# Optimization experiments

Hardware: AMD Instinct MI355X
Metric: run time of the kernel (lower is better)

Reference implementation:

```python
import jax, jax.numpy as jnp
import numpy as np

BETA = 1.0 / np.sqrt(768.0).astype(np.float32)


def setup_inputs() -> dict:
    key = jax.random.key(0)
    k1, k2, k3 = jax.random.split(key, 3)
    x = jax.random.normal(k1, (32, 512, 768), dtype=jnp.float32)
    # torch nn.Linear(dim, n_prototype).weight has shape [n_prototype, dim]
    w_lookup = jax.random.normal(k2, (4096, 768), dtype=jnp.float32) * 0.02
    # torch nn.Linear(n_prototype, dim).weight has shape [dim, n_prototype]
    w_content = jax.random.normal(k3, (768, 4096), dtype=jnp.float32) * 0.02
    return {"x": x, "w_lookup": w_lookup, "w_content": w_content}


def reference(x, w_lookup, w_content):
    # scores: [b, s, n_prototype] = x @ w_lookup^T, scaled by 1/sqrt(dim)
    scores = jnp.einsum("bsd,pd->bsp", x, w_lookup) * jnp.asarray(BETA, x.dtype)
    lookup = jax.nn.softmax(scores, axis=-1)
    # content: [b, s, dim] = lookup @ w_content^T
    content = jnp.einsum("bsp,dp->bsd", lookup, w_content)
    return content  # dropout is identity in eval / p=0.0
```

## Files before the change

### kernel.cpp

```cpp
#include <hip/hip_runtime.h>
#include <hip/hip_bf16.h>


#define NTOK   16384
#define DIM    768
#define NPROT  4096
#define BETA_F 0.03608439182428583f

typedef __bf16 bf16_t;
typedef __bf16 bf16x8 __attribute__((ext_vector_type(8)));
typedef float  floatx4 __attribute__((ext_vector_type(4)));

__device__ __forceinline__ void async_copy16(const bf16_t* g, void* l) {
  __builtin_amdgcn_global_load_lds(
      (__attribute__((address_space(1))) const void*)g,
      (__attribute__((address_space(3))) void*)l, 16, 0, 0);
}

__global__ __launch_bounds__(256) void cvt_all(
    const float* __restrict__ x, const float* __restrict__ wl,
    const float* __restrict__ wc, bf16_t* __restrict__ xb,
    bf16_t* __restrict__ wlb, bf16_t* __restrict__ wcb,
    int nx8, int nw8, int nc8) {
  int i = blockIdx.x * 256 + threadIdx.x;
  const float* in; bf16_t* out; int k;
  if (i < nx8)            { in = x;  out = xb;  k = i; }
  else if (i < nx8 + nw8) { in = wl; out = wlb; k = i - nx8; }
  else if (i < nx8 + nw8 + nc8) { in = wc; out = wcb; k = i - nx8 - nw8; }
  else return;
  const float4* in4 = (const float4*)in;
  float4 a = in4[2 * k], b = in4[2 * k + 1];
  bf16x8 o;
  o[0] = (bf16_t)a.x; o[1] = (bf16_t)a.y; o[2] = (bf16_t)a.z; o[3] = (bf16_t)a.w;
  o[4] = (bf16_t)b.x; o[5] = (bf16_t)b.y; o[6] = (bf16_t)b.z; o[7] = (bf16_t)b.w;
  ((bf16x8*)out)[k] = o;
}

__global__ __launch_bounds__(512, 2)
void gemm256(const bf16_t* __restrict__ A, const bf16_t* __restrict__ B,
             bf16_t* __restrict__ P, float* __restrict__ rowsum,
             const int K, const int N, const int nN) {
  __shared__ char lds[131072];

  const int tid = threadIdx.x;
  const int l   = tid & 63;
  const int w   = tid >> 6;
  const int wr  = w >> 2;
  const int wc  = w & 3;
  const int lr  = l & 15;
  const int lk  = (l >> 4) << 3;

  const int nwg   = gridDim.x;
  const int chunk = nwg >> 3;
  const int wg    = (blockIdx.x & 7) * chunk + (blockIdx.x >> 3);
  const int m0    = (wg / nN) * 256;
  const int n0    = (wg % nN) * 256;

  int aoff[2][2], boff[2][2];
#pragma unroll
  for (int h = 0; h < 2; ++h)
#pragma unroll
    for (int j = 0; j < 2; ++j) {
      const int s     = j * 8 + w;
      const int mfrag = h * 8 + (s >> 1);
      const int ks    = s & 1;
      aoff[h][j] = (m0 + mfrag * 16 + lr) * K + ks * 32 + lk;
      boff[h][j] = (n0 + mfrag * 16 + lr) * K + ks * 32 + lk;
    }

  auto stageA = [&](int slot, int kt, int h) {
#pragma unroll
    for (int j = 0; j < 2; ++j) {
      const int s  = j * 8 + w;
      const int sf = (h * 8 + (s >> 1)) * 2 + (s & 1);
      async_copy16(A + aoff[h][j] + kt * 64, lds + slot * 65536 + sf * 1024);
    }
  };
  auto stageB = [&](int slot, int kt, int h) {
#pragma unroll
    for (int j = 0; j < 2; ++j) {
      const int s  = j * 8 + w;
      const int sf = (h * 8 + (s >> 1)) * 2 + (s & 1);
      async_copy16(B + boff[h][j] + kt * 64,
                   lds + slot * 65536 + 32768 + sf * 1024);
    }
  };

  bf16x8 af[4][2], bg[4][2];
  auto loadA = [&](int slot, int mh) {
#pragma unroll
    for (int q = 0; q < 4; ++q)
#pragma unroll
      for (int ks = 0; ks < 2; ++ks)
        af[q][ks] = *(const bf16x8*)(lds + slot * 65536 +
                        ((mh * 8 + q * 2 + wr) * 2 + ks) * 1024 + l * 16);
  };
  auto loadB = [&](int slot, int nh, int qb) {
#pragma unroll
    for (int q = 0; q < 2; ++q)
#pragma unroll
      for (int ks = 0; ks < 2; ++ks)
        bg[qb + q][ks] = *(const bf16x8*)(lds + slot * 65536 + 32768 +
                        ((nh * 8 + q * 4 + wc) * 2 + ks) * 1024 + l * 16);
  };

  const floatx4 z = {0.f, 0.f, 0.f, 0.f};
  floatx4 acc[8][4];
#pragma unroll
  for (int mt = 0; mt < 8; ++mt)
#pragma unroll
    for (int nt = 0; nt < 4; ++nt) acc[mt][nt] = z;

  auto mma = [&](int mq, int nq) {
    __builtin_amdgcn_s_setprio(1);
#pragma unroll
    for (int q = 0; q < 4; ++q)
#pragma unroll
      for (int r = 0; r < 2; ++r)
#pragma unroll
        for (int ks = 0; ks < 2; ++ks)
          acc[mq * 4 + q][nq * 2 + r] = __builtin_amdgcn_mfma_f32_16x16x32_bf16(
              af[q][ks], bg[nq * 2 + r][ks], acc[mq * 4 + q][nq * 2 + r], 0, 0, 0);
    __builtin_amdgcn_s_setprio(0);
  };

#define BAR()    __builtin_amdgcn_s_barrier()
#define LGKM0()  asm volatile("s_waitcnt lgkmcnt(0)")
#define LGKM8()  asm volatile("s_waitcnt lgkmcnt(8)")
#define VM(n)    asm volatile("s_waitcnt vmcnt(" #n ")" ::: "memory")

  const int T = K >> 6;

  stageA(0, 0, 0); stageB(0, 0, 0); stageB(0, 0, 1); stageA(0, 0, 1);
  stageA(1, 1, 0); stageB(1, 1, 0); stageB(1, 1, 1);
  VM(6);
  BAR();

#pragma unroll 1
  for (int t = 0; t < T - 2; t += 2) {
    loadA(0, 0); loadB(0, 0, 0);
    stageA(1, t + 1, 1);
    LGKM8();
    BAR(); LGKM0(); mma(0, 0); BAR();
    loadB(0, 1, 2);
    stageA(0, t + 2, 0);
    BAR(); LGKM0(); mma(0, 1); BAR();
    loadA(0, 1);
    stageB(0, t + 2, 0);
    BAR(); LGKM0(); mma(1, 1); BAR();
    stageB(0, t + 2, 1);
    BAR(); mma(1, 0); VM(6); BAR();
    loadA(1, 0); loadB(1, 0, 0);
    stageA(0, t + 2, 1);
    LGKM8();
    BAR(); LGKM0(); mma(0, 0); BAR();
    loadB(1, 1, 2);
    stageA(1, t + 3, 0);
    BAR(); LGKM0(); mma(0, 1); BAR();
    loadA(1, 1);
    stageB(1, t + 3, 0);
    BAR(); LGKM0(); mma(1, 1); BAR();
    stageB(1, t + 3, 1);
    BAR(); mma(1, 0); VM(6); BAR();
  }

  loadA(0, 0); loadB(0, 0, 0);
  stageA(1, T - 1, 1);
  LGKM8();
  BAR(); LGKM0(); mma(0, 0); BAR();
  loadB(0, 1, 2);
  BAR(); LGKM0(); mma(0, 1); BAR();
  loadA(0, 1);
  BAR(); LGKM0(); mma(1, 1); BAR();
  BAR(); mma(1, 0); VM(0); BAR();
  loadA(1, 0); loadB(1, 0, 0);
  BAR(); LGKM0(); mma(0, 0); BAR();
  loadB(1, 1, 2);
  BAR(); LGKM0(); mma(0, 1); BAR();
  loadA(1, 1);
  BAR(); LGKM0(); mma(1, 1); BAR();
  mma(1, 0);

  const int hi4 = (l >> 4) << 2;
#pragma unroll
  for (int mt = 0; mt < 8; ++mt) {
    const int row = m0 + (mt * 2 + wr) * 16 + hi4;
    float rs[4] = {0.f, 0.f, 0.f, 0.f};
#pragma unroll
    for (int nt = 0; nt < 4; ++nt) {
      const int col = n0 + (nt * 4 + wc) * 16 + lr;
#pragma unroll
      for (int i = 0; i < 4; ++i) {
        const float e = __expf(acc[mt][nt][i] * BETA_F);
        P[(row + i) * N + col] = (bf16_t)e;
        rs[i] += e;
      }
    }
#pragma unroll
    for (int i = 0; i < 4; ++i) {
      float s = rs[i];
      s += __shfl_xor(s, 1);
      s += __shfl_xor(s, 2);
      s += __shfl_xor(s, 4);
      s += __shfl_xor(s, 8);
      if (lr == 0) atomicAdd(&rowsum[row + i], s);
    }
  }
}

__global__ __launch_bounds__(512, 2)
void gemm192(const bf16_t* __restrict__ A, const bf16_t* __restrict__ B,
             float* __restrict__ O, const float* __restrict__ rowsum,
             const int K, const int N) {
  __shared__ char lds[114688];

  const int tid = threadIdx.x;
  const int l   = tid & 63;
  const int w   = tid >> 6;
  const int wr  = w >> 2;
  const int wc  = w & 3;
  const int lr  = l & 15;
  const int lk  = (l >> 4) << 3;

  const int wg = (blockIdx.x & 7) * 32 + (blockIdx.x >> 3);
  const int m0 = (wg >> 2) * 256;
  const int n0 = (wg & 3) * 192;

  int aoff[2][2];
#pragma unroll
  for (int h = 0; h < 2; ++h)
#pragma unroll
    for (int j = 0; j < 2; ++j) {
      const int s     = j * 8 + w;
      const int mfrag = h * 8 + (s >> 1);
      const int ks    = s & 1;
      aoff[h][j] = (m0 + mfrag * 16 + lr) * K + ks * 32 + lk;
    }
  int boff[3];
#pragma unroll
  for (int t = 0; t < 3; ++t)
    boff[t] = (n0 + (t * 4 + (w >> 1)) * 16 + lr) * K + (w & 1) * 32 + lk;

  auto stageA = [&](int slot, int kt, int h) {
#pragma unroll
    for (int j = 0; j < 2; ++j) {
      const int s  = j * 8 + w;
      const int sf = (h * 8 + (s >> 1)) * 2 + (s & 1);
      async_copy16(A + aoff[h][j] + kt * 64, lds + slot * 57344 + sf * 1024);
    }
  };
  auto stageBt = [&](int slot, int kt, int t) {
    async_copy16(B + boff[t] + kt * 64,
                 lds + slot * 57344 + 32768 + (t * 8 + w) * 1024 + l * 16);
  };

  bf16x8 af[4][2], bg[3][2];
  auto loadA = [&](int slot, int mh) {
#pragma unroll
    for (int q = 0; q < 4; ++q)
#pragma unroll
      for (int ks = 0; ks < 2; ++ks)
        af[q][ks] = *(const bf16x8*)(lds + slot * 57344 +
                        ((mh * 8 + q * 2 + wr) * 2 + ks) * 1024 + l * 16);
  };
  auto loadBn = [&](int slot, int nlo, int ncnt) {
    for (int r = 0; r < ncnt; ++r)
#pragma unroll
      for (int ks = 0; ks < 2; ++ks)
        bg[nlo + r][ks] = *(const bf16x8*)(lds + slot * 57344 + 32768 +
                        (((wc * 3 + nlo + r) * 2 + ks) << 10) + l * 16);
  };

  const floatx4 z = {0.f, 0.f, 0.f, 0.f};
  floatx4 acc[8][3];
#pragma unroll
  for (int mt = 0; mt < 8; ++mt)
#pragma unroll
    for (int nt = 0; nt < 3; ++nt) acc[mt][nt] = z;

  auto mma = [&](int mq, int nlo, int ncnt) {
    __builtin_amdgcn_s_setprio(1);
#pragma unroll
    for (int q = 0; q < 4; ++q)
      for (int r = 0; r < ncnt; ++r)
#pragma unroll
        for (int ks = 0; ks < 2; ++ks)
          acc[mq * 4 + q][nlo + r] = __builtin_amdgcn_mfma_f32_16x16x32_bf16(
              af[q][ks], bg[nlo + r][ks], acc[mq * 4 + q][nlo + r], 0, 0, 0);
    __builtin_amdgcn_s_setprio(0);
  };

  const int T = K >> 6;

  stageA(0, 0, 0); stageA(0, 0, 1);
  stageBt(0, 0, 0); stageBt(0, 0, 1); stageBt(0, 0, 2);
  stageA(1, 1, 0);
  stageBt(1, 1, 0); stageBt(1, 1, 1); stageBt(1, 1, 2);
  VM(5);
  BAR();

#pragma unroll 1
  for (int t = 0; t < T - 2; t += 2) {
#pragma unroll
    for (int u = 0; u < 2; ++u) {
      const int p = u;
      loadA(p, 0); loadBn(p, 0, 2);
      stageA(p ^ 1, t + u + 1, 1);
      LGKM8();
      BAR(); LGKM0(); mma(0, 0, 2); BAR();
      loadBn(p, 2, 1);
      stageA(p, t + u + 2, 0);
      BAR(); LGKM0(); mma(0, 2, 1); BAR();
      loadA(p, 1);
      stageBt(p, t + u + 2, 0); stageBt(p, t + u + 2, 1);
      BAR(); LGKM0(); mma(1, 0, 2); BAR();
      stageBt(p, t + u + 2, 2);
      BAR(); mma(1, 2, 1); VM(5); BAR();
    }
  }

  loadA(0, 0); loadBn(0, 0, 2);
  stageA(1, T - 1, 1);
  LGKM8();
  BAR(); LGKM0(); mma(0, 0, 2); BAR();
  loadBn(0, 2, 1);
  BAR(); LGKM0(); mma(0, 2, 1); BAR();
  loadA(0, 1);
  BAR(); LGKM0(); mma(1, 0, 2); BAR();
  BAR(); mma(1, 2, 1); VM(0); BAR();
  loadA(1, 0); loadBn(1, 0, 2);
  BAR(); LGKM0(); mma(0, 0, 2); BAR();
  loadBn(1, 2, 1);
  BAR(); LGKM0(); mma(0, 2, 1); BAR();
  loadA(1, 1);
  BAR(); LGKM0(); mma(1, 0, 2); BAR();
  mma(1, 2, 1);

#undef BAR
#undef LGKM0
#undef LGKM8
#undef VM

  const int hi4 = (l >> 4) << 2;
#pragma unroll
  for (int mt = 0; mt < 8; ++mt) {
    const int row = m0 + (mt * 2 + wr) * 16 + hi4;
#pragma unroll
    for (int i = 0; i < 4; ++i) {
      const float inv = 1.0f / rowsum[row + i];
#pragma unroll
      for (int nt = 0; nt < 3; ++nt)
        O[(row + i) * N + n0 + (wc * 3 + nt) * 16 + lr] = acc[mt][nt][i] * inv;
    }
  }
}

__global__ __launch_bounds__(256) void hopfield_fallback(
    const float* __restrict__ x, const float* __restrict__ wl,
    const float* __restrict__ wc, float* __restrict__ out) {
  __shared__ float  xs[8 * 768];
  __shared__ bf16_t ps[8 * 4096];
  __shared__ float  rs[8];
  const int tid = threadIdx.x;
  const int r0  = blockIdx.x * 8;
  if (tid < 8) rs[tid] = 0.f;
  for (int i = tid; i < 8 * 768; i += 256)
    xs[i] = x[(r0 + (i / 768)) * 768 + (i % 768)];
  __syncthreads();

  float lsum[8] = {0, 0, 0, 0, 0, 0, 0, 0};
  for (int p = tid; p < 4096; p += 256) {
    float s[8] = {0, 0, 0, 0, 0, 0, 0, 0};
    for (int d = 0; d < 768; ++d) {
      const float wv = wl[p * 768 + d];
#pragma unroll
      for (int r = 0; r < 8; ++r) s[r] += xs[r * 768 + d] * wv;
    }
#pragma unroll
    for (int r = 0; r < 8; ++r) {
      const float e = __expf(s[r] * BETA_F);
      ps[r * 4096 + p] = (bf16_t)e;
      lsum[r] += e;
    }
  }
#pragma unroll
  for (int r = 0; r < 8; ++r) atomicAdd(&rs[r], lsum[r]);
  __syncthreads();

  for (int d = tid; d < 768; d += 256) {
    float o[8] = {0, 0, 0, 0, 0, 0, 0, 0};
    for (int p = 0; p < 4096; ++p) {
      const float wv = wc[d * 4096 + p];
#pragma unroll
      for (int r = 0; r < 8; ++r) o[r] += (float)ps[r * 4096 + p] * wv;
    }
#pragma unroll
    for (int r = 0; r < 8; ++r) out[(r0 + r) * 768 + d] = o[r] / rs[r];
  }
}

extern "C" void kernel_launch(void* const* d_in, const int* in_sizes, int n_in,
                              void* d_out, int out_size, void* d_ws, size_t ws_size,
                              hipStream_t stream) {
  (void)in_sizes; (void)n_in; (void)out_size;
  const float* x  = (const float*)d_in[0];
  const float* wl = (const float*)d_in[1];
  const float* wc = (const float*)d_in[2];
  float* out = (float*)d_out;

  const size_t xb_e = (size_t)NTOK * DIM;
  const size_t wl_e = (size_t)NPROT * DIM;
  const size_t wc_e = (size_t)DIM * NPROT;
  const size_t P_e  = (size_t)NTOK * NPROT;
  const size_t need = (xb_e + wl_e + wc_e + P_e) * 2 + (size_t)NTOK * 4;

  if (ws_size >= need) {
    char* ws = (char*)d_ws;
    bf16_t* xb  = (bf16_t*)ws;  ws += xb_e * 2;
    bf16_t* wlb = (bf16_t*)ws;  ws += wl_e * 2;
    bf16_t* wcb = (bf16_t*)ws;  ws += wc_e * 2;
    bf16_t* P   = (bf16_t*)ws;  ws += P_e * 2;
    float* rowsum = (float*)ws;

    hipMemsetAsync(rowsum, 0, NTOK * sizeof(float), stream);
    const int nx8 = (int)(xb_e / 8), nw8 = (int)(wl_e / 8), nc8 = (int)(wc_e / 8);
    cvt_all<<<(nx8 + nw8 + nc8 + 255) / 256, 256, 0, stream>>>(
        x, wl, wc, xb, wlb, wcb, nx8, nw8, nc8);
    gemm256<<<dim3((NTOK / 256) * (NPROT / 256)), 512, 0, stream>>>(
        xb, wlb, P, rowsum, DIM, NPROT, NPROT / 256);
    gemm192<<<dim3(256), 512, 0, stream>>>(
        P, wcb, out, rowsum, NPROT, DIM);
  } else {
    hopfield_fallback<<<NTOK / 8, 256, 0, stream>>>(x, wl, wc, out);
  }
}
```

Before: 415.0 us.

## Pre-tile bf16 operands into LDS fragment order during conversion for contiguous loads

The fp32-to-bf16 conversion kernel now writes x, w_lookup and w_content in a blocked layout that matches the per-tile LDS fragment order used by both GEMMs. Each async global-to-LDS copy then reads a contiguous 1 KB chunk per fragment instead of 16-byte pieces strided by K. The aim is better memory coalescing and fewer cache lines touched per stage, paid for with scattered writes in the conversion kernel. The layout bakes in the fixed dimensions and tile shapes.

```diff
diff --git a/kernel.cpp b/kernel.cpp
--- a/kernel.cpp
+++ b/kernel.cpp
@@ -23,17 +23,36 @@
     bf16_t* __restrict__ wlb, bf16_t* __restrict__ wcb,
     int nx8, int nw8, int nc8) {
   int i = blockIdx.x * 256 + threadIdx.x;
-  const float* in; bf16_t* out; int k;
-  if (i < nx8)            { in = x;  out = xb;  k = i; }
-  else if (i < nx8 + nw8) { in = wl; out = wlb; k = i - nx8; }
-  else if (i < nx8 + nw8 + nc8) { in = wc; out = wcb; k = i - nx8 - nw8; }
-  else return;
+  const float* in; bf16_t* out; int k; int dv;
+  if (i < nx8) {
+    in = x; out = xb; k = i;
+    const int m = k / 96, kv = k % 96;
+    const int kt = kv >> 3, kr = kv & 7;
+    const int sf = (((m >> 4) & 15) << 1) + (kr >> 2);
+    const int l  = (m & 15) + ((kr & 3) << 4);
+    dv = (((m >> 8) * 12 + kt) * 32 + sf) * 64 + l;
+  } else if (i < nx8 + nw8) {
+    in = wl; out = wlb; k = i - nx8;
+    const int p = k / 96, kv = k % 96;
+    const int kt = kv >> 3, kr = kv & 7;
+    const int sf = (((p >> 4) & 15) << 1) + (kr >> 2);
+    const int l  = (p & 15) + ((kr & 3) << 4);
+    dv = (((p >> 8) * 12 + kt) * 32 + sf) * 64 + l;
+  } else if (i < nx8 + nw8 + nc8) {
+    in = wc; out = wcb; k = i - nx8 - nw8;
+    const int d = k / 512, pv = k % 512;
+    const int kt = pv >> 3, kr = pv & 7;
+    const int dd = d % 192;
+    const int sf = ((dd >> 4) << 1) + (kr >> 2);
+    const int l  = (dd & 15) + ((kr & 3) << 4);
+    dv = (((d / 192) * 64 + kt) * 24 + sf) * 64 + l;
+  } else return;
   const float4* in4 = (const float4*)in;
   float4 a = in4[2 * k], b = in4[2 * k + 1];
   bf16x8 o;
   o[0] = (bf16_t)a.x; o[1] = (bf16_t)a.y; o[2] = (bf16_t)a.z; o[3] = (bf16_t)a.w;
   o[4] = (bf16_t)b.x; o[5] = (bf16_t)b.y; o[6] = (bf16_t)b.z; o[7] = (bf16_t)b.w;
-  ((bf16x8*)out)[k] = o;
+  ((bf16x8*)out)[dv] = o;
 }
 
 __global__ __launch_bounds__(512, 2)
@@ -48,7 +67,6 @@
   const int wr  = w >> 2;
   const int wc  = w & 3;
   const int lr  = l & 15;
-  const int lk  = (l >> 4) << 3;
 
   const int nwg   = gridDim.x;
   const int chunk = nwg >> 3;
@@ -56,16 +74,17 @@
   const int m0    = (wg / nN) * 256;
   const int n0    = (wg % nN) * 256;
 
-  int aoff[2][2], boff[2][2];
+  const int T = K >> 6;
+  const int abase = (m0 >> 8) * T * 16384 + l * 8;
+  const int bbase = (n0 >> 8) * T * 16384 + l * 8;
+  int asf[2][2], bsf[2][2];
 #pragma unroll
   for (int h = 0; h < 2; ++h)
 #pragma unroll
     for (int j = 0; j < 2; ++j) {
-      const int s     = j * 8 + w;
-      const int mfrag = h * 8 + (s >> 1);
-      const int ks    = s & 1;
-      aoff[h][j] = (m0 + mfrag * 16 + lr) * K + ks * 32 + lk;
-      boff[h][j] = (n0 + mfrag * 16 + lr) * K + ks * 32 + lk;
+      const int s = j * 8 + w;
+      asf[h][j] = ((h * 8 + (s >> 1)) * 2 + (s & 1)) * 512;
+      bsf[h][j] = asf[h][j];
     }
 
   auto stageA = [&](int slot, int kt, int h) {
@@ -73,7 +92,8 @@
     for (int j = 0; j < 2; ++j) {
       const int s  = j * 8 + w;
       const int sf = (h * 8 + (s >> 1)) * 2 + (s & 1);
-      async_copy16(A + aoff[h][j] + kt * 64, lds + slot * 65536 + sf * 1024);
+      async_copy16(A + abase + kt * 16384 + asf[h][j],
+                   lds + slot * 65536 + sf * 1024);
     }
   };
   auto stageB = [&](int slot, int kt, int h) {
@@ -81,7 +101,7 @@
     for (int j = 0; j < 2; ++j) {
       const int s  = j * 8 + w;
       const int sf = (h * 8 + (s >> 1)) * 2 + (s & 1);
-      async_copy16(B + boff[h][j] + kt * 64,
+      async_copy16(B + bbase + kt * 16384 + bsf[h][j],
                    lds + slot * 65536 + 32768 + sf * 1024);
     }
   };
@@ -128,8 +148,6 @@
 #define LGKM0()  asm volatile("s_waitcnt lgkmcnt(0)")
 #define LGKM8()  asm volatile("s_waitcnt lgkmcnt(8)")
 #define VM(n)    asm volatile("s_waitcnt vmcnt(" #n ")" ::: "memory")
-
-  const int T = K >> 6;
 
   stageA(0, 0, 0); stageB(0, 0, 0); stageB(0, 0, 1); stageA(0, 0, 1);
   stageA(1, 1, 0); stageB(1, 1, 0); stageB(1, 1, 1);
@@ -236,10 +254,10 @@
       const int ks    = s & 1;
       aoff[h][j] = (m0 + mfrag * 16 + lr) * K + ks * 32 + lk;
     }
-  int boff[3];
-#pragma unroll
-  for (int t = 0; t < 3; ++t)
-    boff[t] = (n0 + (t * 4 + (w >> 1)) * 16 + lr) * K + (w & 1) * 32 + lk;
+  const int bb = (n0 / 192) * 64 * 12288 + l * 8;
+  int bsf[3];
+#pragma unroll
+  for (int t = 0; t < 3; ++t) bsf[t] = (t * 8 + w) * 512;
 
   auto stageA = [&](int slot, int kt, int h) {
 #pragma unroll
@@ -250,7 +268,7 @@
     }
   };
   auto stageBt = [&](int slot, int kt, int t) {
-    async_copy16(B + boff[t] + kt * 64,
+    async_copy16(B + bb + kt * 12288 + bsf[t],
                  lds + slot * 57344 + 32768 + (t * 8 + w) * 1024 + l * 16);
   };
 
```

Result: faster. 385.8 us (-7.0%).
